# Optimization experiments

Measured on AMD Instinct MI355X. Metric: run time of the kernel, lower is better.

## Reference

```python
import jax, jax.numpy as jnp
import numpy as np

N_NODES = 100000
N_INCID = 2000000
HIDDEN = 128
N_HE = 100000


def setup_inputs() -> dict:
    key = jax.random.key(0)
    k1, k2, k3 = jax.random.split(key, 3)
    node_feats = jax.random.normal(k1, (N_NODES, HIDDEN), dtype=jnp.float32)
    hyperedge_index = jax.random.randint(k2, (2, N_INCID), 0, N_HE, dtype=jnp.int64)
    # xavier_uniform for Linear(hidden,1): bound = sqrt(6/(hidden+1))
    bound = float(np.sqrt(6.0 / (HIDDEN + 1)))
    W = jax.random.uniform(k3, (1, HIDDEN), dtype=jnp.float32, minval=-bound, maxval=bound)
    return {"node_feats": node_feats, "hyperedge_index": hyperedge_index,
            "num_hyperedges": N_HE, "W": W}


def reference(node_feats, hyperedge_index, num_hyperedges, W):
    node_idx = hyperedge_index[0]
    he_idx = hyperedge_index[1]
    gathered = node_feats[node_idx]                      # [E, D]
    scores = jnp.einsum('ed,d->e', gathered, W[0])       # [E]
    # segment softmax over hyperedges
    seg_max = jax.ops.segment_max(scores, he_idx, num_segments=num_hyperedges)
    seg_max = jnp.where(jnp.isfinite(seg_max), seg_max, 0.0)  # empty segments
    w = jnp.exp(scores - seg_max[he_idx])                # [E]
    denom = jax.ops.segment_sum(w, he_idx, num_segments=num_hyperedges)
    w_norm = w / jnp.maximum(denom, 1e-20)[he_idx]       # [E]
    # weighted scatter-sum; empty hyperedges stay zero
    out = jax.ops.segment_sum(w_norm[:, None] * gathered, he_idx,
                              num_segments=num_hyperedges)  # [H, D]
    return out
```

## Files before the change

kernel.cpp:

```cpp
#include <hip/hip_runtime.h>
#include <hip/hip_fp16.h>
#include <math.h>

#define N_NODES 100000
#define N_INCID 2000000
#define HIDDEN  128
#define N_HE    100000

#define EPB 1024
#define FILL_BLOCKS ((N_INCID + EPB - 1) / EPB)
#define PREP_BLOCKS ((N_NODES + 3) / 4)

__device__ inline float4 h4_to_f4(uint2 p) {
    __half2 a = *(__half2*)&p.x;
    __half2 b = *(__half2*)&p.y;
    float2 fa = __half22float2(a);
    float2 fb = __half22float2(b);
    return make_float4(fa.x, fa.y, fb.x, fb.y);
}

__global__ void prep_fill_kernel(const float* __restrict__ nf,
                                 const float* __restrict__ W,
                                 const int* __restrict__ idx,
                                 float* __restrict__ en,
                                 __half2* __restrict__ nfh2,
                                 int* __restrict__ counts,
                                 int* __restrict__ csr) {
    int b = blockIdx.x;
    if (b < FILL_BLOCKS) {
        int base = b * EPB;
        int e = base + threadIdx.x;
        if (base + EPB <= N_INCID) {
            int he[4], nd[4], slot[4];
            #pragma unroll
            for (int k = 0; k < 4; ++k) {
                he[k] = idx[N_INCID + e + 256 * k];
                nd[k] = idx[e + 256 * k];
            }
            #pragma unroll
            for (int k = 0; k < 4; ++k) slot[k] = atomicAdd(&counts[he[k]], 1);
            #pragma unroll
            for (int k = 0; k < 4; ++k)
                if (slot[k] < 64) csr[(size_t)he[k] * 64 + slot[k]] = nd[k];
        } else {
            #pragma unroll
            for (int k = 0; k < 4; ++k) {
                int ek = e + 256 * k;
                if (ek < N_INCID) {
                    int he = idx[N_INCID + ek];
                    int nd = idx[ek];
                    int slot = atomicAdd(&counts[he], 1);
                    if (slot < 64) csr[(size_t)he * 64 + slot] = nd;
                }
            }
        }
    } else {
        int wave = threadIdx.x >> 6, lane = threadIdx.x & 63;
        int n = (b - FILL_BLOCKS) * 4 + wave;
        if (n >= N_NODES) return;
        const float2* nf2 = (const float2*)nf;
        const float2* w2  = (const float2*)W;
        float2 v = nf2[(size_t)n * 64 + lane];
        float2 w = w2[lane];
        float p = v.x * w.x + v.y * w.y;
        #pragma unroll
        for (int o = 32; o > 0; o >>= 1) p += __shfl_xor(p, o, 64);
        if (lane == 0) en[n] = __expf(p);
        nfh2[(size_t)n * 64 + lane] = __floats2half2_rn(v.x, v.y);
    }
}

__global__ void compute_kernel_h(const int* __restrict__ counts,
                                 const int* __restrict__ csr,
                                 const float* __restrict__ en,
                                 const uint2* __restrict__ nfh4,
                                 const int* __restrict__ idx,
                                 float* __restrict__ out) {
    int wave = threadIdx.x >> 6, lane = threadIdx.x & 63;
    int he = blockIdx.x * 4 + wave;
    if (he >= N_HE) return;
    int l32 = lane & 31, half = lane >> 5;
    int deg = counts[he];
    float4 acc = make_float4(0.f, 0.f, 0.f, 0.f);

    if (deg <= 64) {
        int nd_l = 0; float e_l = 0.f;
        if (lane < deg) { nd_l = csr[(size_t)he * 64 + lane]; e_l = en[nd_l]; }
        float dsum = e_l;
        #pragma unroll
        for (int o = 32; o > 0; o >>= 1) dsum += __shfl_xor(dsum, o, 64);
        float w_l = e_l * (1.0f / fmaxf(dsum, 1e-20f));

        int degR = (deg + 15) & ~15;
        for (int j = 0; j < degR; j += 16) {
            int   n[8]; float wgt[8]; uint2 p[8];
            #pragma unroll
            for (int k = 0; k < 8; ++k) {
                int r = j + 2 * k + half;
                n[k]   = __shfl(nd_l, r, 64);
                wgt[k] = __shfl(w_l,  r, 64);
            }
            #pragma unroll
            for (int k = 0; k < 8; ++k) p[k] = nfh4[(size_t)n[k] * 32 + l32];
            #pragma unroll
            for (int k = 0; k < 8; ++k) {
                float4 v = h4_to_f4(p[k]);
                acc.x += wgt[k] * v.x; acc.y += wgt[k] * v.y;
                acc.z += wgt[k] * v.z; acc.w += wgt[k] * v.w;
            }
        }
    } else {
        float dsum = 0.f;
        for (int e = lane; e < N_INCID; e += 64)
            if (idx[N_INCID + e] == he) dsum += en[idx[e]];
        #pragma unroll
        for (int o = 32; o > 0; o >>= 1) dsum += __shfl_xor(dsum, o, 64);
        float inv = 1.0f / fmaxf(dsum, 1e-20f);
        for (int e = half; e < N_INCID; e += 2) {
            if (idx[N_INCID + e] == he) {
                int nd = idx[e];
                float w = en[nd] * inv;
                float4 v = h4_to_f4(nfh4[(size_t)nd * 32 + l32]);
                acc.x += w * v.x; acc.y += w * v.y;
                acc.z += w * v.z; acc.w += w * v.w;
            }
        }
    }
    acc.x += __shfl_xor(acc.x, 32, 64);
    acc.y += __shfl_xor(acc.y, 32, 64);
    acc.z += __shfl_xor(acc.z, 32, 64);
    acc.w += __shfl_xor(acc.w, 32, 64);
    if (half == 0) ((float4*)out)[(size_t)he * 32 + l32] = acc;
}

extern "C" void kernel_launch(void* const* d_in, const int* in_sizes, int n_in,
                              void* d_out, int out_size, void* d_ws, size_t ws_size,
                              hipStream_t stream) {
    const float* nf  = (const float*)d_in[0];
    const int*   idx = (const int*)d_in[1];
    const float* W   = (const float*)d_in[3];
    float* out = (float*)d_out;
    char* ws = (char*)d_ws;

    int*     counts = (int*)(ws + 0);
    float*   en     = (float*)(ws + 400000);
    __half2* nfh2   = (__half2*)(ws + 800000);
    int*     csr    = (int*)(ws + 26400000);

    hipMemsetAsync(counts, 0, N_HE * sizeof(int), stream);
    prep_fill_kernel<<<FILL_BLOCKS + PREP_BLOCKS, 256, 0, stream>>>(
        nf, W, idx, en, nfh2, counts, csr);
    compute_kernel_h<<<(N_HE + 3) / 4, 256, 0, stream>>>(
        counts, csr, en, (const uint2*)nfh2, idx, out);
}
```

Measured before the change: 364.8 us.

## Replace bucketed CSR with atomic-exchange linked lists per hyperedge

The fill pass now builds per-hyperedge singly linked lists with atomicExch on a head array plus an (node, next) pair per incidence, replacing the fixed 64-slot bucket CSR and its slow full-scan fallback. The compute kernel gives each half-wave one hyperedge and walks its list serially, accumulating weights and features and normalising at the end. This removes the overflow path and the shuffle broadcasts. In exchange each step waits on a dependent load chain with no batching of independent gathers, so memory-level parallelism per hyperedge drops sharply (about 20 serial hops per hyperedge).

After: 330.9 us. -9.3%, faster.

```diff
diff --git a/kernel.cpp b/kernel.cpp
--- a/kernel.cpp
+++ b/kernel.cpp
@@ -24,24 +24,25 @@
                                  const int* __restrict__ idx,
                                  float* __restrict__ en,
                                  __half2* __restrict__ nfh2,
-                                 int* __restrict__ counts,
-                                 int* __restrict__ csr) {
+                                 int* __restrict__ head,
+                                 int2* __restrict__ next8) {
     int b = blockIdx.x;
     if (b < FILL_BLOCKS) {
         int base = b * EPB;
         int e = base + threadIdx.x;
         if (base + EPB <= N_INCID) {
-            int he[4], nd[4], slot[4];
+            int he[4], nd[4], prev[4];
             #pragma unroll
             for (int k = 0; k < 4; ++k) {
                 he[k] = idx[N_INCID + e + 256 * k];
                 nd[k] = idx[e + 256 * k];
             }
             #pragma unroll
-            for (int k = 0; k < 4; ++k) slot[k] = atomicAdd(&counts[he[k]], 1);
+            for (int k = 0; k < 4; ++k)
+                prev[k] = atomicExch(&head[he[k]], e + 256 * k);
             #pragma unroll
             for (int k = 0; k < 4; ++k)
-                if (slot[k] < 64) csr[(size_t)he[k] * 64 + slot[k]] = nd[k];
+                next8[e + 256 * k] = make_int2(nd[k], prev[k]);
         } else {
             #pragma unroll
             for (int k = 0; k < 4; ++k) {
@@ -49,8 +50,8 @@
                 if (ek < N_INCID) {
                     int he = idx[N_INCID + ek];
                     int nd = idx[ek];
-                    int slot = atomicAdd(&counts[he], 1);
-                    if (slot < 64) csr[(size_t)he * 64 + slot] = nd;
+                    int prev = atomicExch(&head[he], ek);
+                    next8[ek] = make_int2(nd, prev);
                 }
             }
         }
@@ -70,67 +71,31 @@
     }
 }
 
-__global__ void compute_kernel_h(const int* __restrict__ counts,
-                                 const int* __restrict__ csr,
+__global__ void compute_kernel_h(const int* __restrict__ head,
+                                 const int2* __restrict__ next8,
                                  const float* __restrict__ en,
                                  const uint2* __restrict__ nfh4,
-                                 const int* __restrict__ idx,
                                  float* __restrict__ out) {
     int wave = threadIdx.x >> 6, lane = threadIdx.x & 63;
-    int he = blockIdx.x * 4 + wave;
+    int half = lane >> 5, l32 = lane & 31;
+    int he = blockIdx.x * 8 + wave * 2 + half;
     if (he >= N_HE) return;
-    int l32 = lane & 31, half = lane >> 5;
-    int deg = counts[he];
+
     float4 acc = make_float4(0.f, 0.f, 0.f, 0.f);
-
-    if (deg <= 64) {
-        int nd_l = 0; float e_l = 0.f;
-        if (lane < deg) { nd_l = csr[(size_t)he * 64 + lane]; e_l = en[nd_l]; }
-        float dsum = e_l;
-        #pragma unroll
-        for (int o = 32; o > 0; o >>= 1) dsum += __shfl_xor(dsum, o, 64);
-        float w_l = e_l * (1.0f / fmaxf(dsum, 1e-20f));
-
-        int degR = (deg + 15) & ~15;
-        for (int j = 0; j < degR; j += 16) {
-            int   n[8]; float wgt[8]; uint2 p[8];
-            #pragma unroll
-            for (int k = 0; k < 8; ++k) {
-                int r = j + 2 * k + half;
-                n[k]   = __shfl(nd_l, r, 64);
-                wgt[k] = __shfl(w_l,  r, 64);
-            }
-            #pragma unroll
-            for (int k = 0; k < 8; ++k) p[k] = nfh4[(size_t)n[k] * 32 + l32];
-            #pragma unroll
-            for (int k = 0; k < 8; ++k) {
-                float4 v = h4_to_f4(p[k]);
-                acc.x += wgt[k] * v.x; acc.y += wgt[k] * v.y;
-                acc.z += wgt[k] * v.z; acc.w += wgt[k] * v.w;
-            }
-        }
-    } else {
-        float dsum = 0.f;
-        for (int e = lane; e < N_INCID; e += 64)
-            if (idx[N_INCID + e] == he) dsum += en[idx[e]];
-        #pragma unroll
-        for (int o = 32; o > 0; o >>= 1) dsum += __shfl_xor(dsum, o, 64);
-        float inv = 1.0f / fmaxf(dsum, 1e-20f);
-        for (int e = half; e < N_INCID; e += 2) {
-            if (idx[N_INCID + e] == he) {
-                int nd = idx[e];
-                float w = en[nd] * inv;
-                float4 v = h4_to_f4(nfh4[(size_t)nd * 32 + l32]);
-                acc.x += w * v.x; acc.y += w * v.y;
-                acc.z += w * v.z; acc.w += w * v.w;
-            }
-        }
+    float denom = 0.f;
+    int e = head[he];
+    while (e >= 0) {
+        int2 p = next8[e];
+        float w = en[p.x];
+        float4 v = h4_to_f4(nfh4[(size_t)p.x * 32 + l32]);
+        acc.x += w * v.x; acc.y += w * v.y;
+        acc.z += w * v.z; acc.w += w * v.w;
+        denom += w;
+        e = p.y;
     }
-    acc.x += __shfl_xor(acc.x, 32, 64);
-    acc.y += __shfl_xor(acc.y, 32, 64);
-    acc.z += __shfl_xor(acc.z, 32, 64);
-    acc.w += __shfl_xor(acc.w, 32, 64);
-    if (half == 0) ((float4*)out)[(size_t)he * 32 + l32] = acc;
+    float inv = 1.0f / fmaxf(denom, 1e-20f);
+    acc.x *= inv; acc.y *= inv; acc.z *= inv; acc.w *= inv;
+    ((float4*)out)[(size_t)he * 32 + l32] = acc;
 }
 
 extern "C" void kernel_launch(void* const* d_in, const int* in_sizes, int n_in,
@@ -142,14 +107,14 @@
     float* out = (float*)d_out;
     char* ws = (char*)d_ws;
 
-    int*     counts = (int*)(ws + 0);
-    float*   en     = (float*)(ws + 400000);
-    __half2* nfh2   = (__half2*)(ws + 800000);
-    int*     csr    = (int*)(ws + 26400000);
+    int*     head  = (int*)(ws + 0);
+    float*   en    = (float*)(ws + 400000);
+    __half2* nfh2  = (__half2*)(ws + 800000);
+    int2*    next8 = (int2*)(ws + 26400000);
 
-    hipMemsetAsync(counts, 0, N_HE * sizeof(int), stream);
+    hipMemsetAsync(head, 0xFF, N_HE * sizeof(int), stream);
     prep_fill_kernel<<<FILL_BLOCKS + PREP_BLOCKS, 256, 0, stream>>>(
-        nf, W, idx, en, nfh2, counts, csr);
-    compute_kernel_h<<<(N_HE + 3) / 4, 256, 0, stream>>>(
-        counts, csr, en, (const uint2*)nfh2, idx, out);
+        nf, W, idx, en, nfh2, head, next8);
+    compute_kernel_h<<<(N_HE + 7) / 8, 256, 0, stream>>>(
+        head, next8, en, (const uint2*)nfh2, out);
 }
```
